# Kernel tuning notes

Hardware: AMD Instinct MI355X
Metric: run time of the kernel (lower is better)

Reference implementation:

```python
import jax, jax.numpy as jnp
import numpy as np

EMBED_DIM = 128
NUM_SYMBOLS = 200000
B = 1024
K = 200
PROCESS_STEPS = 4


def setup_inputs() -> dict:
    key = jax.random.key(0)
    ks = jax.random.split(key, 10)
    D = EMBED_DIM
    emb = jax.random.normal(ks[0], (NUM_SYMBOLS + 1, D), jnp.float32) * 0.02
    emb = emb.at[NUM_SYMBOLS].set(0.0)  # padding_idx row
    return {
        "relations": jax.random.randint(ks[1], (B, K), 0, NUM_SYMBOLS),
        "entities": jax.random.randint(ks[2], (B, K), 0, NUM_SYMBOLS),
        "query": jax.random.randint(ks[3], (B,), 0, NUM_SYMBOLS),
        "symbol_emb": emb,
        "gcn_w_w": jax.random.normal(ks[4], (D, 2 * D), jnp.float32) / np.sqrt(2 * D).astype(np.float32),
        "gcn_w_b": jnp.zeros((D,), jnp.float32),
        "p1_w": jax.random.normal(ks[5], (2 * D, D), jnp.float32) / np.sqrt(D).astype(np.float32),
        "p1_b": jnp.zeros((2 * D,), jnp.float32),
        "p2_w": jax.random.normal(ks[6], (D, 2 * D), jnp.float32) / np.sqrt(2 * D).astype(np.float32),
        "p2_b": jnp.zeros((D,), jnp.float32),
        "ln_a": jnp.ones((D,), jnp.float32),
        "ln_b": jnp.zeros((D,), jnp.float32),
        "w_ih": jax.random.normal(ks[7], (8 * D, D), jnp.float32) * 0.05,
        "w_hh": jax.random.normal(ks[8], (8 * D, 2 * D), jnp.float32) * 0.05,
        "b_ih": jnp.zeros((8 * D,), jnp.float32),
        "b_hh": jnp.zeros((8 * D,), jnp.float32),
    }


def _layer_norm(z, a, b, eps=1e-3):
    # repo's LayerNormalization: (z - mu) / (std + eps) * a + b, unbiased std
    mu = jnp.mean(z, axis=-1, keepdims=True)
    sigma = jnp.std(z, axis=-1, ddof=1, keepdims=True)
    return (z - mu) / (sigma + eps) * a + b


def _forward(symbol_emb, gcn_w_w, gcn_w_b, p1_w, p1_b, p2_w, p2_b,
             ln_a, ln_b, w_ih, w_hh, b_ih, b_hh,
             relations, entities, query):
    D = symbol_emb.shape[1]
    # --- neighbor_encoder: gather -> concat -> linear -> neighbor sum -> tanh
    rel_e = symbol_emb[relations]                       # (B, K, D)
    ent_e = symbol_emb[entities]                        # (B, K, D)
    concat = jnp.concatenate([rel_e, ent_e], axis=-1)   # (B, K, 2D)
    out = jnp.einsum('bkf,df->bkd', concat, gcn_w_w) + gcn_w_b
    num_neighbors = jnp.asarray(relations.shape[0], out.dtype)  # code uses relations.size()[0]
    support = jnp.tanh(out.sum(axis=1) / num_neighbors)  # (B, D)
    # --- SupportEncoder: FFN with residual + layernorm (dropout off in eval)
    hidden = jax.nn.relu(support @ p1_w.T + p1_b)        # (B, 2D)
    support_g = _layer_norm(hidden @ p2_w.T + p2_b + support, ln_a, ln_b)
    # --- QueryEncoder: LSTMCell(D, 2D) process block with attention over support
    q = symbol_emb[query]                                # (B, D)
    bsz = q.shape[0]
    h_r = jnp.zeros((bsz, 2 * D), q.dtype)
    c = jnp.zeros((bsz, 2 * D), q.dtype)
    h_out = q
    for _ in range(PROCESS_STEPS):
        gates = q @ w_ih.T + b_ih + h_r @ w_hh.T + b_hh  # (B, 8D)
        i, f, g, o = jnp.split(gates, 4, axis=-1)
        c = jax.nn.sigmoid(f) * c + jax.nn.sigmoid(i) * jnp.tanh(g)
        h_ = jax.nn.sigmoid(o) * jnp.tanh(c)             # (B, 2D)
        h_out = q + h_[:, :D]                            # (B, D)
        attn = jax.nn.softmax(h_out @ support_g.T, axis=1)  # (B, B)
        r = attn @ support_g                             # (B, D)
        h_r = jnp.concatenate([h_out, r], axis=-1)       # (B, 2D)
    query_embeds = h_out
    # --- cosine similarity over dim=1
    cross = jnp.sum(query_embeds * support_g, axis=1)
    n1 = jnp.sum(query_embeds * query_embeds, axis=1)
    n2 = jnp.sum(support_g * support_g, axis=1)
    return cross / jnp.sqrt(n1 * n2)                     # (B,)


def reference(relations, entities, query, symbol_emb, gcn_w_w, gcn_w_b,
              p1_w, p1_b, p2_w, p2_b, ln_a, ln_b, w_ih, w_hh, b_ih, b_hh):
    return _forward(symbol_emb, gcn_w_w, gcn_w_b, p1_w, p1_b, p2_w, p2_b,
                    ln_a, ln_b, w_ih, w_hh, b_ih, b_hh,
                    relations, entities, query)
```

## Files before the change

kernel.cpp:

```cpp
#include <hip/hip_runtime.h>
#include <math.h>

#define D 128
#define TWO_D 256
#define B_SZ 1024
#define KNB 200
#define AW 392

typedef _Float16 half8 __attribute__((ext_vector_type(8)));
typedef _Float16 half4 __attribute__((ext_vector_type(4)));
typedef float floatx4 __attribute__((ext_vector_type(4)));

__device__ __forceinline__ float sigmoid_f(float x) { return 1.f / (1.f + __expf(-x)); }
__device__ __forceinline__ float tanh_fast(float x) { return 1.f - 2.f / (__expf(2.f * x) + 1.f); }

__global__ __launch_bounds__(256) void k_support(
    const int* __restrict__ relations, const int* __restrict__ entities,
    const int* __restrict__ query, const float* __restrict__ emb,
    const float* __restrict__ gcn_w, const float* __restrict__ gcn_b,
    const float* __restrict__ p1_w, const float* __restrict__ p1_b,
    const float* __restrict__ p2_w, const float* __restrict__ p2_b,
    const float* __restrict__ ln_a, const float* __restrict__ ln_b,
    float* __restrict__ sg, _Float16* __restrict__ sgH, _Float16* __restrict__ sgT,
    float* __restrict__ qbuf, _Float16* __restrict__ qbH)
{
    __shared__ int idxs[2 * KNB];
    __shared__ __align__(16) float part[8][132];
    __shared__ __align__(16) float S[TWO_D];
    __shared__ __align__(16) float sup[D];
    __shared__ __align__(16) float hid[TWO_D];
    __shared__ __align__(16) float zv[D];
    __shared__ float red2[2];

    const int b = blockIdx.x;
    const int t = threadIdx.x;

    for (int i = t; i < KNB; i += 256) idxs[i] = relations[b * KNB + i];
    for (int i = t; i < KNB; i += 256) idxs[KNB + i] = entities[b * KNB + i];
    __syncthreads();

    {
        const int g = t >> 5, c4 = (t & 31) * 4;
        const int* mi = &idxs[(g >> 2) * KNB];
        float4 a4 = make_float4(0.f, 0.f, 0.f, 0.f);
        #pragma unroll 10
        for (int k = (g & 3); k < KNB; k += 4) {
            float4 v = *(const float4*)&emb[(size_t)mi[k] * D + c4];
            a4.x += v.x; a4.y += v.y; a4.z += v.z; a4.w += v.w;
        }
        *(float4*)&part[g][c4] = a4;
    }
    __syncthreads();
    {
        const int half = t >> 7, c = t & 127;
        const float* p = &part[half * 4][0];
        S[t] = (p[c] + p[132 + c]) + (p[264 + c] + p[396 + c]);
    }
    __syncthreads();

    if (t < D) {
        const float4* w4 = (const float4*)(gcn_w + t * TWO_D);
        float dot = 0.f;
        #pragma unroll 8
        for (int f = 0; f < TWO_D / 4; ++f) {
            float4 w = w4[f];
            float4 s = *(const float4*)&S[f * 4];
            dot += w.x * s.x + w.y * s.y + w.z * s.z + w.w * s.w;
        }
        float v = (dot + 200.f * gcn_b[t]) * (1.f / 1024.f);
        sup[t] = tanhf(v);
    }
    __syncthreads();

    {
        const float4* w4 = (const float4*)(p1_w + t * D);
        float dot = 0.f;
        #pragma unroll 8
        for (int f = 0; f < D / 4; ++f) {
            float4 w = w4[f];
            float4 s = *(const float4*)&sup[f * 4];
            dot += w.x * s.x + w.y * s.y + w.z * s.z + w.w * s.w;
        }
        float h = dot + p1_b[t];
        hid[t] = h > 0.f ? h : 0.f;
    }
    __syncthreads();

    if (t < D) {
        const float4* w4 = (const float4*)(p2_w + t * TWO_D);
        float dot = 0.f;
        #pragma unroll 8
        for (int f = 0; f < TWO_D / 4; ++f) {
            float4 w = w4[f];
            float4 s = *(const float4*)&hid[f * 4];
            dot += w.x * s.x + w.y * s.y + w.z * s.z + w.w * s.w;
        }
        zv[t] = dot + p2_b[t] + sup[t];
    }
    __syncthreads();

    if (t < 64) {
        float x0 = zv[t], x1 = zv[t + 64];
        float s = x0 + x1;
        for (int off = 32; off; off >>= 1) s += __shfl_down(s, off);
        float mu = __shfl(s, 0) * (1.f / 128.f);
        float d0 = x0 - mu, d1 = x1 - mu;
        float v = d0 * d0 + d1 * d1;
        for (int off = 32; off; off >>= 1) v += __shfl_down(v, off);
        v = __shfl(v, 0);
        if (t == 0) { red2[0] = mu; red2[1] = sqrtf(v * (1.f / 127.f)); }
    }
    __syncthreads();
    if (t < D) {
        float mu = red2[0], sigma = red2[1];
        float val = (zv[t] - mu) / (sigma + 1e-3f) * ln_a[t] + ln_b[t];
        sg[b * D + t] = val;
        sgH[b * D + t] = (_Float16)val;
        sgT[t * B_SZ + b] = (_Float16)val;
        float qv = emb[(size_t)query[b] * D + t];
        qbuf[b * D + t] = qv;
        qbH[b * D + t] = (_Float16)qv;
    }
}

__global__ __launch_bounds__(256) void k_gates_mfma(
    const _Float16* __restrict__ qbH, const _Float16* __restrict__ hH,
    const _Float16* __restrict__ rbH,
    const float* __restrict__ w_ih, const float* __restrict__ w_hh,
    const float* __restrict__ b_ih, const float* __restrict__ b_hh,
    const float* __restrict__ qb,
    float* __restrict__ cbuf, float* __restrict__ hout,
    _Float16* __restrict__ houtH, int kend, int first)
{
    __shared__ _Float16 Ah[64 * AW];
    __shared__ _Float16 Bh[2][4][16][40];

    const int t = threadIdx.x;
    const int b0 = blockIdx.x * 64;
    const int n0 = blockIdx.y * 16;
    const int lane = t & 63, wv = t >> 6;
    const int m = lane & 15, quad = lane >> 4;

    {
        const int row = t >> 2;
        const int gr = b0 + row;
        for (int c4 = (t & 3) * 4; c4 < kend; c4 += 16) {
            const _Float16* src;
            if (c4 < 128)      src = &qbH[gr * D + c4];
            else if (c4 < 256) src = &hH[gr * D + (c4 - 128)];
            else               src = &rbH[gr * D + (c4 - 256)];
            *(half4*)&Ah[row * AW + c4] = *(const half4*)src;
        }
    }

    const int sg_g = t >> 6, sg_u = (t >> 2) & 15, sg_kq = (t & 3) * 8;
    auto stage_b = [&](int ks, int buf) {
        const int grow = sg_g * 256 + n0 + sg_u;
        const int k0 = ks * 32 + sg_kq;
        const float* src = (k0 < 128) ? &w_ih[grow * D + k0]
                                      : &w_hh[grow * TWO_D + (k0 - 128)];
        float4 v0 = *(const float4*)src;
        float4 v1 = *(const float4*)(src + 4);
        half8 h;
        h[0] = (_Float16)v0.x; h[1] = (_Float16)v0.y; h[2] = (_Float16)v0.z; h[3] = (_Float16)v0.w;
        h[4] = (_Float16)v1.x; h[5] = (_Float16)v1.y; h[6] = (_Float16)v1.z; h[7] = (_Float16)v1.w;
        *(half8*)&Bh[buf][sg_g][sg_u][sg_kq] = h;
    };

    stage_b(0, 0);
    __syncthreads();

    floatx4 acc[4];
    #pragma unroll
    for (int g = 0; g < 4; ++g)
        #pragma unroll
        for (int i = 0; i < 4; ++i) acc[g][i] = 0.f;

    const int nsteps = kend >> 5;
    for (int ks = 0; ks < nsteps; ++ks) {
        if (ks + 1 < nsteps) stage_b(ks + 1, (ks + 1) & 1);
        half8 a = *(const half8*)&Ah[(wv * 16 + m) * AW + ks * 32 + quad * 8];
        #pragma unroll
        for (int g = 0; g < 4; ++g) {
            half8 bf = *(const half8*)&Bh[ks & 1][g][m][quad * 8];
            acc[g] = __builtin_amdgcn_mfma_f32_16x16x32_f16(a, bf, acc[g], 0, 0, 0);
        }
        __syncthreads();
    }

    const int unit = n0 + m;
    float bi[4];
    #pragma unroll
    for (int g = 0; g < 4; ++g) bi[g] = b_ih[g * 256 + unit] + b_hh[g * 256 + unit];
    #pragma unroll
    for (int rr = 0; rr < 4; ++rr) {
        const int b = b0 + wv * 16 + quad * 4 + rr;
        float gi = acc[0][rr] + bi[0];
        float gf = acc[1][rr] + bi[1];
        float gg = acc[2][rr] + bi[2];
        float go = acc[3][rr] + bi[3];
        float cold = first ? 0.f : cbuf[b * TWO_D + unit];
        float cnew = sigmoid_f(gf) * cold + sigmoid_f(gi) * tanh_fast(gg);
        cbuf[b * TWO_D + unit] = cnew;
        if (n0 < D) {
            float h = sigmoid_f(go) * tanh_fast(cnew);
            float ho = qb[b * D + unit] + h;
            hout[b * D + unit] = ho;
            houtH[b * D + unit] = (_Float16)ho;
        }
    }
}

__global__ __launch_bounds__(256) void k_scores_mfma(
    const _Float16* __restrict__ hH, const _Float16* __restrict__ sgH,
    float* __restrict__ scores)
{
    const int t = threadIdx.x;
    const int lane = t & 63, wv = t >> 6;
    const int m = lane & 15, quad = lane >> 4;
    const int b0 = blockIdx.x * 64, j0 = blockIdx.y * 64;
    const int arow = b0 + wv * 16 + m;

    floatx4 acc[4];
    #pragma unroll
    for (int nt = 0; nt < 4; ++nt)
        #pragma unroll
        for (int i = 0; i < 4; ++i) acc[nt][i] = 0.f;

    #pragma unroll
    for (int ks = 0; ks < 4; ++ks) {
        const int k0 = ks * 32 + quad * 8;
        half8 a = *(const half8*)&hH[arow * D + k0];
        #pragma unroll
        for (int nt = 0; nt < 4; ++nt) {
            half8 bf = *(const half8*)&sgH[(j0 + nt * 16 + m) * D + k0];
            acc[nt] = __builtin_amdgcn_mfma_f32_16x16x32_f16(a, bf, acc[nt], 0, 0, 0);
        }
    }
    #pragma unroll
    for (int nt = 0; nt < 4; ++nt)
        #pragma unroll
        for (int rr = 0; rr < 4; ++rr)
            scores[(b0 + wv * 16 + quad * 4 + rr) * B_SZ + j0 + nt * 16 + m] = acc[nt][rr];
}

__global__ __launch_bounds__(256) void k_stats(
    const float* __restrict__ scores, float2* __restrict__ stats)
{
    __shared__ float red[4];
    __shared__ float smx;
    const int b = blockIdx.x, t = threadIdx.x;
    const float* row = scores + b * B_SZ;
    float v0 = row[t], v1 = row[t + 256], v2 = row[t + 512], v3 = row[t + 768];
    float m = fmaxf(fmaxf(v0, v1), fmaxf(v2, v3));
    for (int off = 32; off; off >>= 1) m = fmaxf(m, __shfl_down(m, off));
    if ((t & 63) == 0) red[t >> 6] = m;
    __syncthreads();
    if (t == 0) smx = fmaxf(fmaxf(red[0], red[1]), fmaxf(red[2], red[3]));
    __syncthreads();
    const float mx = smx;
    float s = __expf(v0 - mx) + __expf(v1 - mx) + __expf(v2 - mx) + __expf(v3 - mx);
    for (int off = 32; off; off >>= 1) s += __shfl_down(s, off);
    __syncthreads();
    if ((t & 63) == 0) red[t >> 6] = s;
    __syncthreads();
    if (t == 0) stats[b] = make_float2(mx, 1.f / (red[0] + red[1] + red[2] + red[3]));
}

__global__ __launch_bounds__(256) void k_rgemm_mfma(
    const float* __restrict__ scores, const float2* __restrict__ stats,
    const _Float16* __restrict__ sgT, float* __restrict__ rpart)
{
    const int t = threadIdx.x;
    const int wv = t >> 6, lane = t & 63;
    const int m = lane & 15, quad = lane >> 4;
    const int m0 = blockIdx.x * 16;
    const int kbase = blockIdx.y * 128;
    const float2 st = stats[m0 + m];

    floatx4 acc[2];
    #pragma unroll
    for (int nt = 0; nt < 2; ++nt)
        #pragma unroll
        for (int i = 0; i < 4; ++i) acc[nt][i] = 0.f;

    #pragma unroll
    for (int ks = 0; ks < 4; ++ks) {
        const int k0 = kbase + ks * 32 + quad * 8;
        const float* sp = &scores[(m0 + m) * B_SZ + k0];
        float4 v0 = *(const float4*)sp;
        float4 v1 = *(const float4*)(sp + 4);
        half8 a;
        a[0] = (_Float16)(__expf(v0.x - st.x) * st.y);
        a[1] = (_Float16)(__expf(v0.y - st.x) * st.y);
        a[2] = (_Float16)(__expf(v0.z - st.x) * st.y);
        a[3] = (_Float16)(__expf(v0.w - st.x) * st.y);
        a[4] = (_Float16)(__expf(v1.x - st.x) * st.y);
        a[5] = (_Float16)(__expf(v1.y - st.x) * st.y);
        a[6] = (_Float16)(__expf(v1.z - st.x) * st.y);
        a[7] = (_Float16)(__expf(v1.w - st.x) * st.y);
        #pragma unroll
        for (int nt = 0; nt < 2; ++nt) {
            const int col0 = (wv * 2 + nt) * 16;
            half8 bf = *(const half8*)&sgT[(col0 + m) * B_SZ + k0];
            acc[nt] = __builtin_amdgcn_mfma_f32_16x16x32_f16(a, bf, acc[nt], 0, 0, 0);
        }
    }
    float* rp = rpart + blockIdx.y * (B_SZ * D);
    #pragma unroll
    for (int nt = 0; nt < 2; ++nt)
        #pragma unroll
        for (int rr = 0; rr < 4; ++rr)
            rp[(m0 + quad * 4 + rr) * D + (wv * 2 + nt) * 16 + m] = acc[nt][rr];
}

__global__ __launch_bounds__(256) void k_rreduce(
    const float* __restrict__ rpart, _Float16* __restrict__ rbH)
{
    const int i = (blockIdx.x * 256 + threadIdx.x) * 4;
    float4 s = *(const float4*)&rpart[i];
    #pragma unroll
    for (int j = 1; j < 8; ++j) {
        float4 v = *(const float4*)&rpart[j * (B_SZ * D) + i];
        s.x += v.x; s.y += v.y; s.z += v.z; s.w += v.w;
    }
    half4 h;
    h[0] = (_Float16)s.x; h[1] = (_Float16)s.y;
    h[2] = (_Float16)s.z; h[3] = (_Float16)s.w;
    *(half4*)&rbH[i] = h;
}

__global__ __launch_bounds__(64) void k_cosine(
    const float* __restrict__ hout, const float* __restrict__ sg,
    float* __restrict__ out)
{
    const int b = blockIdx.x, t = threadIdx.x;
    float a0 = hout[b * D + t], a1 = hout[b * D + t + 64];
    float s0 = sg[b * D + t], s1 = sg[b * D + t + 64];
    float cr = a0 * s0 + a1 * s1;
    float n1 = a0 * a0 + a1 * a1;
    float n2 = s0 * s0 + s1 * s1;
    for (int off = 32; off; off >>= 1) {
        cr += __shfl_down(cr, off);
        n1 += __shfl_down(n1, off);
        n2 += __shfl_down(n2, off);
    }
    if (t == 0) out[b] = cr / sqrtf(n1 * n2);
}

extern "C" void kernel_launch(void* const* d_in, const int* in_sizes, int n_in,
                              void* d_out, int out_size, void* d_ws, size_t ws_size,
                              hipStream_t stream)
{
    const int*   relations = (const int*)d_in[0];
    const int*   entities  = (const int*)d_in[1];
    const int*   query     = (const int*)d_in[2];
    const float* emb       = (const float*)d_in[3];
    const float* gcn_w     = (const float*)d_in[4];
    const float* gcn_b     = (const float*)d_in[5];
    const float* p1_w      = (const float*)d_in[6];
    const float* p1_b      = (const float*)d_in[7];
    const float* p2_w      = (const float*)d_in[8];
    const float* p2_b      = (const float*)d_in[9];
    const float* ln_a      = (const float*)d_in[10];
    const float* ln_b      = (const float*)d_in[11];
    const float* w_ih      = (const float*)d_in[12];
    const float* w_hh      = (const float*)d_in[13];
    const float* b_ih      = (const float*)d_in[14];
    const float* b_hh      = (const float*)d_in[15];

    float* ws = (float*)d_ws;
    float*     sg     = ws;
    float*     qb     = ws + 131072;
    float*     hoA    = ws + 262144;
    float*     hoB    = ws + 393216;
    float*     cb     = ws + 524288;
    float*     scores = ws + 786432;
    float*     rpart  = ws + 1835008;
    float2*    stats  = (float2*)(ws + 2883584);
    _Float16*  sgH    = (_Float16*)(ws + 2885632);
    _Float16*  sgT    = (_Float16*)(ws + 2951168);
    _Float16*  qbH    = (_Float16*)(ws + 3016704);
    _Float16*  hHA    = (_Float16*)(ws + 3082240);
    _Float16*  hHB    = (_Float16*)(ws + 3147776);
    _Float16*  rbH    = (_Float16*)(ws + 3213312);

    k_support<<<dim3(B_SZ), dim3(256), 0, stream>>>(
        relations, entities, query, emb, gcn_w, gcn_b,
        p1_w, p1_b, p2_w, p2_b, ln_a, ln_b, sg, sgH, sgT, qb, qbH);

    k_gates_mfma<<<dim3(16, 16), dim3(256), 0, stream>>>(
        qbH, hHA, rbH, w_ih, w_hh, b_ih, b_hh, qb, cb, hoB, hHB, 128, 1);
    k_scores_mfma<<<dim3(16, 16), dim3(256), 0, stream>>>(hHB, sgH, scores);
    k_stats<<<dim3(B_SZ), dim3(256), 0, stream>>>(scores, stats);
    k_rgemm_mfma<<<dim3(64, 8), dim3(256), 0, stream>>>(scores, stats, sgT, rpart);
    k_rreduce<<<dim3(128), dim3(256), 0, stream>>>(rpart, rbH);

    k_gates_mfma<<<dim3(16, 16), dim3(256), 0, stream>>>(
        qbH, hHB, rbH, w_ih, w_hh, b_ih, b_hh, qb, cb, hoA, hHA, 384, 0);
    k_scores_mfma<<<dim3(16, 16), dim3(256), 0, stream>>>(hHA, sgH, scores);
    k_stats<<<dim3(B_SZ), dim3(256), 0, stream>>>(scores, stats);
    k_rgemm_mfma<<<dim3(64, 8), dim3(256), 0, stream>>>(scores, stats, sgT, rpart);
    k_rreduce<<<dim3(128), dim3(256), 0, stream>>>(rpart, rbH);

    k_gates_mfma<<<dim3(16, 16), dim3(256), 0, stream>>>(
        qbH, hHA, rbH, w_ih, w_hh, b_ih, b_hh, qb, cb, hoB, hHB, 384, 0);
    k_scores_mfma<<<dim3(16, 16), dim3(256), 0, stream>>>(hHB, sgH, scores);
    k_stats<<<dim3(B_SZ), dim3(256), 0, stream>>>(scores, stats);
    k_rgemm_mfma<<<dim3(64, 8), dim3(256), 0, stream>>>(scores, stats, sgT, rpart);
    k_rreduce<<<dim3(128), dim3(256), 0, stream>>>(rpart, rbH);

    k_gates_mfma<<<dim3(16, 16), dim3(256), 0, stream>>>(
        qbH, hHB, rbH, w_ih, w_hh, b_ih, b_hh, qb, cb, hoA, hHA, 384, 0);

    k_cosine<<<dim3(B_SZ), dim3(64), 0, stream>>>(hoA, sg, (float*)d_out);
}
```

Baseline: 338.1 us.

## Fuse softmax stats and split-K reduce into neighbors, preconvert LSTM weights to fp16

Removes the separate softmax-stats and partial-sum reduce kernels. Each rgemm block now computes row max and sum itself, and the gates kernel sums the split-K partials while staging its A tile. The LSTM weights are converted to fp16 once up front instead of being converted in every gates launch, split-K drops from 8 to 4, and the support kernel uses 512 threads for the gather. This cuts launch count and global round trips, at the cost of each rgemm block recomputing full-row stats redundantly across its split-K blocks.

After: 319.2 us. 5.6% less time.

```diff
diff --git a/kernel.cpp b/kernel.cpp
--- a/kernel.cpp
+++ b/kernel.cpp
@@ -6,6 +6,7 @@
 #define B_SZ 1024
 #define KNB 200
 #define AW 392
+#define NKC 4
 
 typedef _Float16 half8 __attribute__((ext_vector_type(8)));
 typedef _Float16 half4 __attribute__((ext_vector_type(4)));
@@ -14,7 +15,21 @@
 __device__ __forceinline__ float sigmoid_f(float x) { return 1.f / (1.f + __expf(-x)); }
 __device__ __forceinline__ float tanh_fast(float x) { return 1.f - 2.f / (__expf(2.f * x) + 1.f); }
 
-__global__ __launch_bounds__(256) void k_support(
+__global__ __launch_bounds__(256) void k_cvtw(
+    const float* __restrict__ w_ih, const float* __restrict__ w_hh,
+    _Float16* __restrict__ w16)
+{
+    const int i8 = (blockIdx.x * 256 + threadIdx.x) * 8;
+    const float* src = (i8 < 131072) ? (w_ih + i8) : (w_hh + (i8 - 131072));
+    float4 v0 = *(const float4*)src;
+    float4 v1 = *(const float4*)(src + 4);
+    half8 h;
+    h[0] = (_Float16)v0.x; h[1] = (_Float16)v0.y; h[2] = (_Float16)v0.z; h[3] = (_Float16)v0.w;
+    h[4] = (_Float16)v1.x; h[5] = (_Float16)v1.y; h[6] = (_Float16)v1.z; h[7] = (_Float16)v1.w;
+    *(half8*)&w16[i8] = h;
+}
+
+__global__ __launch_bounds__(512) void k_support(
     const int* __restrict__ relations, const int* __restrict__ entities,
     const int* __restrict__ query, const float* __restrict__ emb,
     const float* __restrict__ gcn_w, const float* __restrict__ gcn_b,
@@ -25,7 +40,7 @@
     float* __restrict__ qbuf, _Float16* __restrict__ qbH)
 {
     __shared__ int idxs[2 * KNB];
-    __shared__ __align__(16) float part[8][132];
+    __shared__ __align__(16) float part[16][132];
     __shared__ __align__(16) float S[TWO_D];
     __shared__ __align__(16) float sup[D];
     __shared__ __align__(16) float hid[TWO_D];
@@ -35,26 +50,28 @@
     const int b = blockIdx.x;
     const int t = threadIdx.x;
 
-    for (int i = t; i < KNB; i += 256) idxs[i] = relations[b * KNB + i];
-    for (int i = t; i < KNB; i += 256) idxs[KNB + i] = entities[b * KNB + i];
+    if (t < KNB) idxs[t] = relations[b * KNB + t];
+    else if (t < 2 * KNB) idxs[t] = entities[b * KNB + (t - KNB)];
     __syncthreads();
 
     {
         const int g = t >> 5, c4 = (t & 31) * 4;
-        const int* mi = &idxs[(g >> 2) * KNB];
+        const int* mi = &idxs[(g >> 3) * KNB];
         float4 a4 = make_float4(0.f, 0.f, 0.f, 0.f);
-        #pragma unroll 10
-        for (int k = (g & 3); k < KNB; k += 4) {
+        #pragma unroll 5
+        for (int k = (g & 7); k < KNB; k += 8) {
             float4 v = *(const float4*)&emb[(size_t)mi[k] * D + c4];
             a4.x += v.x; a4.y += v.y; a4.z += v.z; a4.w += v.w;
         }
         *(float4*)&part[g][c4] = a4;
     }
     __syncthreads();
-    {
+    if (t < TWO_D) {
         const int half = t >> 7, c = t & 127;
-        const float* p = &part[half * 4][0];
-        S[t] = (p[c] + p[132 + c]) + (p[264 + c] + p[396 + c]);
+        float s = 0.f;
+        #pragma unroll
+        for (int j = 0; j < 8; ++j) s += part[half * 8 + j][c];
+        S[t] = s;
     }
     __syncthreads();
 
@@ -72,7 +89,7 @@
     }
     __syncthreads();
 
-    {
+    if (t < TWO_D) {
         const float4* w4 = (const float4*)(p1_w + t * D);
         float dot = 0.f;
         #pragma unroll 8
@@ -125,8 +142,7 @@
 
 __global__ __launch_bounds__(256) void k_gates_mfma(
     const _Float16* __restrict__ qbH, const _Float16* __restrict__ hH,
-    const _Float16* __restrict__ rbH,
-    const float* __restrict__ w_ih, const float* __restrict__ w_hh,
+    const float* __restrict__ rpart, const _Float16* __restrict__ w16,
     const float* __restrict__ b_ih, const float* __restrict__ b_hh,
     const float* __restrict__ qb,
     float* __restrict__ cbuf, float* __restrict__ hout,
@@ -145,11 +161,23 @@
         const int row = t >> 2;
         const int gr = b0 + row;
         for (int c4 = (t & 3) * 4; c4 < kend; c4 += 16) {
-            const _Float16* src;
-            if (c4 < 128)      src = &qbH[gr * D + c4];
-            else if (c4 < 256) src = &hH[gr * D + (c4 - 128)];
-            else               src = &rbH[gr * D + (c4 - 256)];
-            *(half4*)&Ah[row * AW + c4] = *(const half4*)src;
+            half4 h;
+            if (c4 < 128) {
+                h = *(const half4*)&qbH[gr * D + c4];
+            } else if (c4 < 256) {
+                h = *(const half4*)&hH[gr * D + (c4 - 128)];
+            } else {
+                const int c = c4 - 256;
+                float4 s4 = *(const float4*)&rpart[gr * D + c];
+                #pragma unroll
+                for (int j = 1; j < NKC; ++j) {
+                    float4 v = *(const float4*)&rpart[j * (B_SZ * D) + gr * D + c];
+                    s4.x += v.x; s4.y += v.y; s4.z += v.z; s4.w += v.w;
+                }
+                h[0] = (_Float16)s4.x; h[1] = (_Float16)s4.y;
+                h[2] = (_Float16)s4.z; h[3] = (_Float16)s4.w;
+            }
+            *(half4*)&Ah[row * AW + c4] = h;
         }
     }
 
@@ -157,14 +185,9 @@
     auto stage_b = [&](int ks, int buf) {
         const int grow = sg_g * 256 + n0 + sg_u;
         const int k0 = ks * 32 + sg_kq;
-        const float* src = (k0 < 128) ? &w_ih[grow * D + k0]
-                                      : &w_hh[grow * TWO_D + (k0 - 128)];
-        float4 v0 = *(const float4*)src;
-        float4 v1 = *(const float4*)(src + 4);
-        half8 h;
-        h[0] = (_Float16)v0.x; h[1] = (_Float16)v0.y; h[2] = (_Float16)v0.z; h[3] = (_Float16)v0.w;
-        h[4] = (_Float16)v1.x; h[5] = (_Float16)v1.y; h[6] = (_Float16)v1.z; h[7] = (_Float16)v1.w;
-        *(half8*)&Bh[buf][sg_g][sg_u][sg_kq] = h;
+        const _Float16* src = (k0 < 128) ? &w16[grow * D + k0]
+                                         : &w16[131072 + grow * TWO_D + (k0 - 128)];
+        *(half8*)&Bh[buf][sg_g][sg_u][sg_kq] = *(const half8*)src;
     };
 
     stage_b(0, 0);
@@ -244,39 +267,41 @@
             scores[(b0 + wv * 16 + quad * 4 + rr) * B_SZ + j0 + nt * 16 + m] = acc[nt][rr];
 }
 
-__global__ __launch_bounds__(256) void k_stats(
-    const float* __restrict__ scores, float2* __restrict__ stats)
-{
-    __shared__ float red[4];
-    __shared__ float smx;
-    const int b = blockIdx.x, t = threadIdx.x;
-    const float* row = scores + b * B_SZ;
-    float v0 = row[t], v1 = row[t + 256], v2 = row[t + 512], v3 = row[t + 768];
-    float m = fmaxf(fmaxf(v0, v1), fmaxf(v2, v3));
-    for (int off = 32; off; off >>= 1) m = fmaxf(m, __shfl_down(m, off));
-    if ((t & 63) == 0) red[t >> 6] = m;
-    __syncthreads();
-    if (t == 0) smx = fmaxf(fmaxf(red[0], red[1]), fmaxf(red[2], red[3]));
-    __syncthreads();
-    const float mx = smx;
-    float s = __expf(v0 - mx) + __expf(v1 - mx) + __expf(v2 - mx) + __expf(v3 - mx);
-    for (int off = 32; off; off >>= 1) s += __shfl_down(s, off);
-    __syncthreads();
-    if ((t & 63) == 0) red[t >> 6] = s;
-    __syncthreads();
-    if (t == 0) stats[b] = make_float2(mx, 1.f / (red[0] + red[1] + red[2] + red[3]));
-}
-
 __global__ __launch_bounds__(256) void k_rgemm_mfma(
-    const float* __restrict__ scores, const float2* __restrict__ stats,
-    const _Float16* __restrict__ sgT, float* __restrict__ rpart)
-{
+    const float* __restrict__ scores, const _Float16* __restrict__ sgT,
+    float* __restrict__ rpart)
+{
+    __shared__ float st_lds[16][2];
+
     const int t = threadIdx.x;
     const int wv = t >> 6, lane = t & 63;
     const int m = lane & 15, quad = lane >> 4;
     const int m0 = blockIdx.x * 16;
-    const int kbase = blockIdx.y * 128;
-    const float2 st = stats[m0 + m];
+    const int kbase = blockIdx.y * (B_SZ / NKC);
+
+    #pragma unroll
+    for (int r = 0; r < 4; ++r) {
+        const int row = m0 + wv * 4 + r;
+        const float* sp = &scores[row * B_SZ + lane * 16];
+        float4 c0 = *(const float4*)sp;
+        float4 c1 = *(const float4*)(sp + 4);
+        float4 c2 = *(const float4*)(sp + 8);
+        float4 c3 = *(const float4*)(sp + 12);
+        float mm = fmaxf(fmaxf(fmaxf(c0.x, c0.y), fmaxf(c0.z, c0.w)),
+                  fmaxf(fmaxf(fmaxf(c1.x, c1.y), fmaxf(c1.z, c1.w)),
+                  fmaxf(fmaxf(fmaxf(c2.x, c2.y), fmaxf(c2.z, c2.w)),
+                        fmaxf(fmaxf(c3.x, c3.y), fmaxf(c3.z, c3.w)))));
+        for (int off = 32; off; off >>= 1) mm = fmaxf(mm, __shfl_down(mm, off));
+        mm = __shfl(mm, 0);
+        float ss = __expf(c0.x - mm) + __expf(c0.y - mm) + __expf(c0.z - mm) + __expf(c0.w - mm)
+                 + __expf(c1.x - mm) + __expf(c1.y - mm) + __expf(c1.z - mm) + __expf(c1.w - mm)
+                 + __expf(c2.x - mm) + __expf(c2.y - mm) + __expf(c2.z - mm) + __expf(c2.w - mm)
+                 + __expf(c3.x - mm) + __expf(c3.y - mm) + __expf(c3.z - mm) + __expf(c3.w - mm);
+        for (int off = 32; off; off >>= 1) ss += __shfl_down(ss, off);
+        if (lane == 0) { st_lds[wv * 4 + r][0] = mm; st_lds[wv * 4 + r][1] = 1.f / ss; }
+    }
+    __syncthreads();
+    const float stx = st_lds[m][0], sty = st_lds[m][1];
 
     floatx4 acc[2];
     #pragma unroll
@@ -285,20 +310,20 @@
         for (int i = 0; i < 4; ++i) acc[nt][i] = 0.f;
 
     #pragma unroll
-    for (int ks = 0; ks < 4; ++ks) {
+    for (int ks = 0; ks < (B_SZ / NKC) / 32; ++ks) {
         const int k0 = kbase + ks * 32 + quad * 8;
         const float* sp = &scores[(m0 + m) * B_SZ + k0];
         float4 v0 = *(const float4*)sp;
         float4 v1 = *(const float4*)(sp + 4);
         half8 a;
-        a[0] = (_Float16)(__expf(v0.x - st.x) * st.y);
-        a[1] = (_Float16)(__expf(v0.y - st.x) * st.y);
-        a[2] = (_Float16)(__expf(v0.z - st.x) * st.y);
-        a[3] = (_Float16)(__expf(v0.w - st.x) * st.y);
-        a[4] = (_Float16)(__expf(v1.x - st.x) * st.y);
-        a[5] = (_Float16)(__expf(v1.y - st.x) * st.y);
-        a[6] = (_Float16)(__expf(v1.z - st.x) * st.y);
-        a[7] = (_Float16)(__expf(v1.w - st.x) * st.y);
+        a[0] = (_Float16)(__expf(v0.x - stx) * sty);
+        a[1] = (_Float16)(__expf(v0.y - stx) * sty);
+        a[2] = (_Float16)(__expf(v0.z - stx) * sty);
+        a[3] = (_Float16)(__expf(v0.w - stx) * sty);
+        a[4] = (_Float16)(__expf(v1.x - stx) * sty);
+        a[5] = (_Float16)(__expf(v1.y - stx) * sty);
+        a[6] = (_Float16)(__expf(v1.z - stx) * sty);
+        a[7] = (_Float16)(__expf(v1.w - stx) * sty);
         #pragma unroll
         for (int nt = 0; nt < 2; ++nt) {
             const int col0 = (wv * 2 + nt) * 16;
@@ -312,22 +337,6 @@
         #pragma unroll
         for (int rr = 0; rr < 4; ++rr)
             rp[(m0 + quad * 4 + rr) * D + (wv * 2 + nt) * 16 + m] = acc[nt][rr];
-}
-
-__global__ __launch_bounds__(256) void k_rreduce(
-    const float* __restrict__ rpart, _Float16* __restrict__ rbH)
-{
-    const int i = (blockIdx.x * 256 + threadIdx.x) * 4;
-    float4 s = *(const float4*)&rpart[i];
-    #pragma unroll
-    for (int j = 1; j < 8; ++j) {
-        float4 v = *(const float4*)&rpart[j * (B_SZ * D) + i];
-        s.x += v.x; s.y += v.y; s.z += v.z; s.w += v.w;
-    }
-    half4 h;
-    h[0] = (_Float16)s.x; h[1] = (_Float16)s.y;
-    h[2] = (_Float16)s.z; h[3] = (_Float16)s.w;
-    *(half4*)&rbH[i] = h;
 }
 
 __global__ __launch_bounds__(64) void k_cosine(
@@ -377,41 +386,35 @@
     float*     cb     = ws + 524288;
     float*     scores = ws + 786432;
     float*     rpart  = ws + 1835008;
-    float2*    stats  = (float2*)(ws + 2883584);
-    _Float16*  sgH    = (_Float16*)(ws + 2885632);
-    _Float16*  sgT    = (_Float16*)(ws + 2951168);
-    _Float16*  qbH    = (_Float16*)(ws + 3016704);
-    _Float16*  hHA    = (_Float16*)(ws + 3082240);
-    _Float16*  hHB    = (_Float16*)(ws + 3147776);
-    _Float16*  rbH    = (_Float16*)(ws + 3213312);
-
-    k_support<<<dim3(B_SZ), dim3(256), 0, stream>>>(
+    _Float16*  sgH    = (_Float16*)(ws + 2359296);
+    _Float16*  sgT    = (_Float16*)(ws + 2424832);
+    _Float16*  qbH    = (_Float16*)(ws + 2490368);
+    _Float16*  hHA    = (_Float16*)(ws + 2555904);
+    _Float16*  hHB    = (_Float16*)(ws + 2621440);
+    _Float16*  w16    = (_Float16*)(ws + 2686976);
+
+    k_cvtw<<<dim3(192), dim3(256), 0, stream>>>(w_ih, w_hh, w16);
+    k_support<<<dim3(B_SZ), dim3(512), 0, stream>>>(
         relations, entities, query, emb, gcn_w, gcn_b,
         p1_w, p1_b, p2_w, p2_b, ln_a, ln_b, sg, sgH, sgT, qb, qbH);
 
     k_gates_mfma<<<dim3(16, 16), dim3(256), 0, stream>>>(
-        qbH, hHA, rbH, w_ih, w_hh, b_ih, b_hh, qb, cb, hoB, hHB, 128, 1);
+        qbH, hHA, rpart, w16, b_ih, b_hh, qb, cb, hoB, hHB, 128, 1);
     k_scores_mfma<<<dim3(16, 16), dim3(256), 0, stream>>>(hHB, sgH, scores);
-    k_stats<<<dim3(B_SZ), dim3(256), 0, stream>>>(scores, stats);
-    k_rgemm_mfma<<<dim3(64, 8), dim3(256), 0, stream>>>(scores, stats, sgT, rpart);
-    k_rreduce<<<dim3(128), dim3(256), 0, stream>>>(rpart, rbH);
+    k_rgemm_mfma<<<dim3(64, NKC), dim3(256), 0, stream>>>(scores, sgT, rpart);
 
     k_gates_mfma<<<dim3(16, 16), dim3(256), 0, stream>>>(
-        qbH, hHB, rbH, w_ih, w_hh, b_ih, b_hh, qb, cb, hoA, hHA, 384, 0);
+        qbH, hHB, rpart, w16, b_ih, b_hh, qb, cb, hoA, hHA, 384, 0);
     k_scores_mfma<<<dim3(16, 16), dim3(256), 0, stream>>>(hHA, sgH, scores);
-    k_stats<<<dim3(B_SZ), dim3(256), 0, stream>>>(scores, stats);
-    k_rgemm_mfma<<<dim3(64, 8), dim3(256), 0, stream>>>(scores, stats, sgT, rpart);
-    k_rreduce<<<dim3(128), dim3(256), 0, stream>>>(rpart, rbH);
+    k_rgemm_mfma<<<dim3(64, NKC), dim3(256), 0, stream>>>(scores, sgT, rpart);
 
     k_gates_mfma<<<dim3(16, 16), dim3(256), 0, stream>>>(
-        qbH, hHA, rbH, w_ih, w_hh, b_ih, b_hh, qb, cb, hoB, hHB, 384, 0);
+        qbH, hHA, rpart, w16, b_ih, b_hh, qb, cb, hoB, hHB, 384, 0);
     k_scores_mfma<<<dim3(16, 16), dim3(256), 0, stream>>>(hHB, sgH, scores);
-    k_stats<<<dim3(B_SZ), dim3(256), 0, stream>>>(scores, stats);
-    k_rgemm_mfma<<<dim3(64, 8), dim3(256), 0, stream>>>(scores, stats, sgT, rpart);
-    k_rreduce<<<dim3(128), dim3(256), 0, stream>>>(rpart, rbH);
+    k_rgemm_mfma<<<dim3(64, NKC), dim3(256), 0, stream>>>(scores, sgT, rpart);
 
     k_gates_mfma<<<dim3(16, 16), dim3(256), 0, stream>>>(
-        qbH, hHB, rbH, w_ih, w_hh, b_ih, b_hh, qb, cb, hoA, hHA, 384, 0);
+        qbH, hHB, rpart, w16, b_ih, b_hh, qb, cb, hoA, hHA, 384, 0);
 
     k_cosine<<<dim3(B_SZ), dim3(64), 0, stream>>>(hoA, sg, (float*)d_out);
 }
```
